# Optimization experiments

Hardware: AMD Instinct MI355X
Metric: run time of the kernel (lower is better)

## Reference

```python
import jax, jax.numpy as jnp
import numpy as np

B, T, C, NH = 4, 2048, 1024, 16
HS = C // NH


def setup_inputs() -> dict:
    key = jax.random.key(0)
    k1, k2, k3, k4, k5 = jax.random.split(key, 5)
    s = 1.0 / np.sqrt(C)
    return {
        "x": jax.random.normal(k1, (B, T, C), dtype=jnp.float32),
        "Wqkv": jax.random.normal(k2, (3 * C, C), dtype=jnp.float32) * s,
        "bqkv": jax.random.normal(k3, (3 * C,), dtype=jnp.float32) * 0.02,
        "Wproj": jax.random.normal(k4, (C, C), dtype=jnp.float32) * s,
        "bproj": jax.random.normal(k5, (C,), dtype=jnp.float32) * 0.02,
    }


def reference(x, Wqkv, bqkv, Wproj, bproj):
    Bsz, Tlen, Cdim = x.shape
    # qkv projection (torch Linear: x @ W.T + b)
    qkv = x @ Wqkv.T + bqkv                      # [B, T, 3C]
    q, k, v = jnp.split(qkv, 3, axis=-1)
    # [B, NH, T, HS]
    q = q.reshape(Bsz, Tlen, NH, HS).transpose(0, 2, 1, 3)
    k = k.reshape(Bsz, Tlen, NH, HS).transpose(0, 2, 1, 3)
    v = v.reshape(Bsz, Tlen, NH, HS).transpose(0, 2, 1, 3)
    scale = 1.0 / np.sqrt(HS)
    att = jnp.einsum('bhqd,bhkd->bhqk', q, k) * scale
    causal = jnp.triu(jnp.ones((Tlen, Tlen), dtype=bool), k=1)
    att = jnp.where(causal[None, None], -jnp.inf, att)
    att = jax.nn.softmax(att, axis=-1)
    y = jnp.einsum('bhqk,bhkd->bhqd', att, v)    # [B, NH, T, HS]
    y = y.transpose(0, 2, 1, 3).reshape(Bsz, Tlen, Cdim)
    return y @ Wproj.T + bproj
```

## Files before the change

kernel.cpp:

```cpp
#include <hip/hip_runtime.h>
#include <hip/hip_bf16.h>

#define B_   4
#define T_   2048
#define C_   1024
#define NH_  16
#define HS_  64
#define M_   8192
#define N1_  3072
#define BH_  64

typedef __attribute__((ext_vector_type(8))) short short8;
typedef __attribute__((ext_vector_type(4))) short short4v;
typedef __attribute__((ext_vector_type(4))) float f32x4;

#define QSCALE 0.18033688011112042f

__device__ __forceinline__ short f2bf(float f) {
  unsigned u = __float_as_uint(f);
  unsigned r = (u + 0x7fffu + ((u >> 16) & 1u)) >> 16;
  return (short)r;
}
__device__ __forceinline__ unsigned pk_bf16(float a, float b) {
  __hip_bfloat162 h = __float22bfloat162_rn(make_float2(a, b));
  union { __hip_bfloat162 h2; unsigned u; } cv; cv.h2 = h; return cv.u;
}

typedef __attribute__((address_space(1))) unsigned int as1_uint;
typedef __attribute__((address_space(3))) unsigned int as3_uint;
__device__ __forceinline__ void g2l16(const void* g, void* l) {
  __builtin_amdgcn_global_load_lds((as1_uint*)g, (as3_uint*)l, 16, 0, 0);
}

__global__ __launch_bounds__(256) void conv_bf16(
    const float* __restrict__ src, short* __restrict__ dst)
{
  const size_t i = ((size_t)blockIdx.x * 256 + threadIdx.x) * 8;
  const f32x4 a = *(const f32x4*)&src[i];
  const f32x4 b = *(const f32x4*)&src[i + 4];
  short8 o;
  o[0] = f2bf(a[0]); o[1] = f2bf(a[1]); o[2] = f2bf(a[2]); o[3] = f2bf(a[3]);
  o[4] = f2bf(b[0]); o[5] = f2bf(b[1]); o[6] = f2bf(b[2]); o[7] = f2bf(b[3]);
  *(short8*)&dst[i] = o;
}

#define NT_ 32

#define GEMM_PRELUDE() \
  const int tid = threadIdx.x; \
  const int lane = tid & 63; \
  const int wid = tid >> 6; \
  const int wy = wid >> 1, wx = wid & 1; \
  const int lq = lane >> 4, lm = lane & 15; \
  const int row0 = blockIdx.x * 128; \
  const int col0 = blockIdx.y * 128; \
  f32x4 acc[4][4] = {}; \
  const int s0 = tid, s1 = tid + 256;             \
  const int r0 = s0 >> 2, r1 = s1 >> 2;           \
  const int c0s = ((s0 & 3) ^ ((r0 >> 1) & 3)) * 8;   \
  const int c1s = ((s1 & 3) ^ ((r1 >> 1) & 3)) * 8; \
  const int rsw = (lq ^ ((lm >> 1) & 3)) * 8;

#define GEMM_STAGE(PA, PB, k0, bi) do { \
    g2l16(&PA[(size_t)(row0 + r0) * C_ + (k0) + c0s], &As[bi][s0 * 8]); \
    g2l16(&PA[(size_t)(row0 + r1) * C_ + (k0) + c1s], &As[bi][s1 * 8]); \
    g2l16(&PB[(size_t)(col0 + r0) * C_ + (k0) + c0s], &Bs[bi][s0 * 8]); \
    g2l16(&PB[(size_t)(col0 + r1) * C_ + (k0) + c1s], &Bs[bi][s1 * 8]); \
  } while (0)

#define GEMM_MAINLOOP(PA, PB) \
  GEMM_STAGE(PA, PB, 0, 0); \
  GEMM_STAGE(PA, PB, 32, 1); \
  int cur = 0; \
  for (int t = 0; t < NT_; ++t) { \
    if (t < NT_ - 1) { asm volatile("s_waitcnt vmcnt(4)" ::: "memory"); } \
    else             { asm volatile("s_waitcnt vmcnt(0)" ::: "memory"); } \
    __builtin_amdgcn_sched_barrier(0); \
    __builtin_amdgcn_s_barrier(); \
    __builtin_amdgcn_sched_barrier(0); \
    { \
      const short* Ab = &As[cur][0]; \
      const short* Bb = &Bs[cur][0]; \
      short8 af[4], bfr[4]; \
      _Pragma("unroll") \
      for (int mi = 0; mi < 4; ++mi) \
        af[mi] = *(const short8*)&Ab[(wy * 64 + mi * 16 + lm) * 32 + rsw]; \
      _Pragma("unroll") \
      for (int ni = 0; ni < 4; ++ni) \
        bfr[ni] = *(const short8*)&Bb[(wx * 64 + ni * 16 + lm) * 32 + rsw]; \
      _Pragma("unroll") \
      for (int mi = 0; mi < 4; ++mi) \
        _Pragma("unroll") \
        for (int ni = 0; ni < 4; ++ni) \
          acc[mi][ni] = __builtin_amdgcn_mfma_f32_16x16x32_bf16(af[mi], bfr[ni], acc[mi][ni], 0, 0, 0); \
    } \
    if (t + 2 < NT_) { \
      const int bi2 = (cur + 2) - ((cur + 2) >= 3 ? 3 : 0); \
      GEMM_STAGE(PA, PB, (t + 2) * 32, bi2); \
    } \
    cur = (cur + 1) - ((cur + 1) >= 3 ? 3 : 0); \
  }

__global__ __launch_bounds__(256) void qkv_gemm(
    const short* __restrict__ X,
    const short* __restrict__ W,
    const float* __restrict__ bias,
    short* __restrict__ Qo, short* __restrict__ Ko, short* __restrict__ Vt)
{
  __shared__ short As[3][128 * 32];
  __shared__ short Bs[3][128 * 32];
  GEMM_PRELUDE();
  GEMM_MAINLOOP(X, W);

#pragma unroll
  for (int ni = 0; ni < 4; ++ni) {
    const int n = col0 + wx * 64 + ni * 16 + lm;
    const float bv = bias[n];
    const int sel = n >> 10;
    const int cc = n & (C_ - 1);
    const int h = cc >> 6, d = cc & 63;
    if (sel == 2) {
#pragma unroll
      for (int mi = 0; mi < 4; ++mi) {
        const int m0 = row0 + wy * 64 + mi * 16 + lq * 4;
        const int b = m0 >> 11, t0 = m0 & (T_ - 1);
        const int bh = b * NH_ + h;
        short4v o;
#pragma unroll
        for (int i = 0; i < 4; ++i) o[i] = f2bf(acc[mi][ni][i] + bv);
        *(short4v*)&Vt[((size_t)bh * HS_ + d) * T_ + t0] = o;
      }
    } else {
      short* dst = (sel == 0) ? Qo : Ko;
      const float qs = (sel == 0) ? QSCALE : 1.0f;
#pragma unroll
      for (int mi = 0; mi < 4; ++mi) {
#pragma unroll
        for (int i = 0; i < 4; ++i) {
          const int m = row0 + wy * 64 + mi * 16 + lq * 4 + i;
          const int b = m >> 11, t = m & (T_ - 1);
          const int bh = b * NH_ + h;
          dst[((size_t)bh * T_ + t) * HS_ + d] = f2bf((acc[mi][ni][i] + bv) * qs);
        }
      }
    }
  }
}

__global__ __launch_bounds__(256) void proj_gemm(
    const short* __restrict__ Y,
    const short* __restrict__ W,
    const float* __restrict__ bias,
    float* __restrict__ Out)
{
  __shared__ short As[3][128 * 32];
  __shared__ short Bs[3][128 * 32];
  GEMM_PRELUDE();
  GEMM_MAINLOOP(Y, W);

#pragma unroll
  for (int ni = 0; ni < 4; ++ni) {
    const int n = col0 + wx * 64 + ni * 16 + lm;
    const float bv = bias[n];
#pragma unroll
    for (int mi = 0; mi < 4; ++mi) {
#pragma unroll
      for (int i = 0; i < 4; ++i) {
        const int m = row0 + wy * 64 + mi * 16 + lq * 4 + i;
        Out[(size_t)m * C_ + n] = acc[mi][ni][i] + bv;
      }
    }
  }
}

#define LDK 72
__global__ __launch_bounds__(512, 4) void attn(
    const short* __restrict__ Qg, const short* __restrict__ Kg,
    const short* __restrict__ Vg, short* __restrict__ Yo)
{
  __shared__ short Ks[64 * LDK];
  __shared__ short Vs[64 * LDK];

  const int tid = threadIdx.x;
  const int lane = tid & 63;
  const int w = tid >> 6;
  const int wq = w & 3;
  const int grp = w >> 2;
  const int lq = lane >> 4, lm = lane & 15;
  const int bh = blockIdx.x;
  const int b = bh >> 4, h = bh & 15;
  const size_t base = (size_t)bh * T_ * HS_;
  const short* __restrict__ Kb = Kg + base;
  const short* __restrict__ Vb = Vg + base;

  const int sr = tid >> 3;
  const int sc = (tid & 7) * 8;

  const int ty = blockIdx.y;
  const int qt = grp ? ty : (15 - ty);
  const int nkt_g = 2 * qt + 2;
  const int nktA = 32 - 2 * ty;

  const int qA = qt * 128 + wq * 16 + lm;
  const int qB = qA + 64;

  const short8 qfA0 = *(const short8*)&Qg[base + (size_t)qA * HS_ + lq * 8];
  const short8 qfA1 = *(const short8*)&Qg[base + (size_t)qA * HS_ + 32 + lq * 8];
  const short8 qfB0 = *(const short8*)&Qg[base + (size_t)qB * HS_ + lq * 8];
  const short8 qfB1 = *(const short8*)&Qg[base + (size_t)qB * HS_ + 32 + lq * 8];

  float lA = 0.0f, lB = 0.0f;
  f32x4 oA[4] = {}, oB[4] = {};

  short8 pk = *(const short8*)&Kb[(size_t)sr * HS_ + sc];
  short8 pv = *(const short8*)&Vb[(size_t)sr * T_ + sc];

#pragma unroll 1
  for (int kt = 0; kt < nktA; ++kt) {
    const int kv0 = kt * 64;

    __syncthreads();
    *(short8*)&Ks[sr * LDK + sc] = pk;
    *(short8*)&Vs[sr * LDK + sc] = pv;
    __syncthreads();

    if (kt + 1 < nktA) {
      pk = *(const short8*)&Kb[(size_t)(kv0 + 64 + sr) * HS_ + sc];
      pv = *(const short8*)&Vb[(size_t)sr * T_ + kv0 + 64 + sc];
    }

    if (kt < nkt_g) {
      const bool doA = (kt <= 2 * qt);

      short8 kf0[4], kf1[4];
#pragma unroll
      for (int ni = 0; ni < 4; ++ni) {
        kf0[ni] = *(const short8*)&Ks[(ni * 16 + lm) * LDK + lq * 8];
        kf1[ni] = *(const short8*)&Ks[(ni * 16 + lm) * LDK + 32 + lq * 8];
      }

      f32x4 svA[4], svB[4];
      if (doA) {
#pragma unroll
        for (int ni = 0; ni < 4; ++ni) {
          f32x4 s = {};
          s = __builtin_amdgcn_mfma_f32_16x16x32_bf16(kf0[ni], qfA0, s, 0, 0, 0);
          svA[ni] = __builtin_amdgcn_mfma_f32_16x16x32_bf16(kf1[ni], qfA1, s, 0, 0, 0);
        }
      }
#pragma unroll
      for (int ni = 0; ni < 4; ++ni) {
        f32x4 s = {};
        s = __builtin_amdgcn_mfma_f32_16x16x32_bf16(kf0[ni], qfB0, s, 0, 0, 0);
        svB[ni] = __builtin_amdgcn_mfma_f32_16x16x32_bf16(kf1[ni], qfB1, s, 0, 0, 0);
      }

      if (kt == 2 * qt) {
#pragma unroll
        for (int ni = 0; ni < 4; ++ni) {
          const int kvb = kv0 + ni * 16 + lq * 4;
#pragma unroll
          for (int i = 0; i < 4; ++i)
            if (kvb + i > qA) svA[ni][i] = -3.0e38f;
        }
      }
      if (kt == 2 * qt + 1) {
#pragma unroll
        for (int ni = 0; ni < 4; ++ni) {
          const int kvb = kv0 + ni * 16 + lq * 4;
#pragma unroll
          for (int i = 0; i < 4; ++i)
            if (kvb + i > qB) svB[ni][i] = -3.0e38f;
        }
      }

      short4v p4A[4], p4B[4];
      if (doA) {
#pragma unroll
        for (int ni = 0; ni < 4; ++ni)
#pragma unroll
          for (int i = 0; i < 4; ++i)
            svA[ni][i] = __builtin_amdgcn_exp2f(svA[ni][i]);
        lA += ((svA[0][0] + svA[0][1]) + (svA[0][2] + svA[0][3]))
            + ((svA[1][0] + svA[1][1]) + (svA[1][2] + svA[1][3]))
            + ((svA[2][0] + svA[2][1]) + (svA[2][2] + svA[2][3]))
            + ((svA[3][0] + svA[3][1]) + (svA[3][2] + svA[3][3]));
#pragma unroll
        for (int ni = 0; ni < 4; ++ni) {
          union { short4v s4; unsigned u[2]; } pk2;
          pk2.u[0] = pk_bf16(svA[ni][0], svA[ni][1]);
          pk2.u[1] = pk_bf16(svA[ni][2], svA[ni][3]);
          p4A[ni] = pk2.s4;
        }
      }
#pragma unroll
      for (int ni = 0; ni < 4; ++ni)
#pragma unroll
        for (int i = 0; i < 4; ++i)
          svB[ni][i] = __builtin_amdgcn_exp2f(svB[ni][i]);
      lB += ((svB[0][0] + svB[0][1]) + (svB[0][2] + svB[0][3]))
          + ((svB[1][0] + svB[1][1]) + (svB[1][2] + svB[1][3]))
          + ((svB[2][0] + svB[2][1]) + (svB[2][2] + svB[2][3]))
          + ((svB[3][0] + svB[3][1]) + (svB[3][2] + svB[3][3]));
#pragma unroll
      for (int ni = 0; ni < 4; ++ni) {
        union { short4v s4; unsigned u[2]; } pk2;
        pk2.u[0] = pk_bf16(svB[ni][0], svB[ni][1]);
        pk2.u[1] = pk_bf16(svB[ni][2], svB[ni][3]);
        p4B[ni] = pk2.s4;
      }

      if (doA) {
#pragma unroll
        for (int di = 0; di < 4; ++di) {
#pragma unroll
          for (int ni = 0; ni < 4; ++ni) {
            const short4v vfr = *(const short4v*)&Vs[(di * 16 + lm) * LDK + ni * 16 + lq * 4];
            oA[di] = __builtin_amdgcn_mfma_f32_16x16x16bf16_1k(vfr, p4A[ni], oA[di], 0, 0, 0);
            oB[di] = __builtin_amdgcn_mfma_f32_16x16x16bf16_1k(vfr, p4B[ni], oB[di], 0, 0, 0);
          }
        }
      } else {
#pragma unroll
        for (int di = 0; di < 4; ++di) {
#pragma unroll
          for (int ni = 0; ni < 4; ++ni) {
            const short4v vfr = *(const short4v*)&Vs[(di * 16 + lm) * LDK + ni * 16 + lq * 4];
            oB[di] = __builtin_amdgcn_mfma_f32_16x16x16bf16_1k(vfr, p4B[ni], oB[di], 0, 0, 0);
          }
        }
      }
    }
  }

  lA += __shfl_xor(lA, 16);
  lA += __shfl_xor(lA, 32);
  lB += __shfl_xor(lB, 16);
  lB += __shfl_xor(lB, 32);
  const float rlA = 1.0f / lA;
  const float rlB = 1.0f / lB;
  const size_t rowA = ((size_t)(b * T_ + qA)) * C_ + h * HS_;
  const size_t rowB = ((size_t)(b * T_ + qB)) * C_ + h * HS_;
#pragma unroll
  for (int di = 0; di < 4; ++di) {
    union { short4v s4; unsigned u[2]; } pk2;
    pk2.u[0] = pk_bf16(oA[di][0] * rlA, oA[di][1] * rlA);
    pk2.u[1] = pk_bf16(oA[di][2] * rlA, oA[di][3] * rlA);
    *(short4v*)&Yo[rowA + di * 16 + lq * 4] = pk2.s4;
    pk2.u[0] = pk_bf16(oB[di][0] * rlB, oB[di][1] * rlB);
    pk2.u[1] = pk_bf16(oB[di][2] * rlB, oB[di][3] * rlB);
    *(short4v*)&Yo[rowB + di * 16 + lq * 4] = pk2.s4;
  }
}

extern "C" void kernel_launch(void* const* d_in, const int* in_sizes, int n_in,
                              void* d_out, int out_size, void* d_ws, size_t ws_size,
                              hipStream_t stream) {
  (void)in_sizes; (void)n_in; (void)out_size;
  const float* x     = (const float*)d_in[0];
  const float* Wqkv  = (const float*)d_in[1];
  const float* bqkv  = (const float*)d_in[2];
  const float* Wproj = (const float*)d_in[3];
  const float* bproj = (const float*)d_in[4];
  float* out = (float*)d_out;

  const size_t nWq = (size_t)N1_ * C_;
  const size_t nWp = (size_t)C_ * C_;
  const size_t nFull = (size_t)M_ * C_;
  const size_t nB = (size_t)T_ * C_;

  dim3 blk(256);
  const size_t need_batched = (nWq + nWp + 4 * nFull) * sizeof(short);

  if (ws_size >= need_batched) {
    short* Wq_bf = (short*)d_ws;
    short* Wp_bf = Wq_bf + nWq;
    short* S0    = Wp_bf + nWp;
    short* Qw    = S0 + nFull;
    short* Kw    = Qw + nFull;
    short* Vw    = Kw + nFull;

    conv_bf16<<<dim3((int)(nWq / 2048)), blk, 0, stream>>>(Wqkv, Wq_bf);
    conv_bf16<<<dim3((int)(nWp / 2048)), blk, 0, stream>>>(Wproj, Wp_bf);
    conv_bf16<<<dim3((int)(nFull / 2048)), blk, 0, stream>>>(x, S0);
    qkv_gemm<<<dim3(M_ / 128, N1_ / 128), blk, 0, stream>>>(S0, Wq_bf, bqkv, Qw, Kw, Vw);
    attn<<<dim3(BH_, 8), dim3(512), 0, stream>>>(Qw, Kw, Vw, S0);
    proj_gemm<<<dim3(M_ / 128, C_ / 128), blk, 0, stream>>>(S0, Wp_bf, bproj, out);
  } else {
    short* Wq_bf = (short*)d_ws;
    short* Wp_bf = Wq_bf + nWq;
    short* S0    = Wp_bf + nWp;
    short* Qw    = S0 + nB;
    short* Kw    = Qw + nB;
    short* Vw    = Kw + nB;

    conv_bf16<<<dim3((int)(nWq / 2048)), blk, 0, stream>>>(Wqkv, Wq_bf);
    conv_bf16<<<dim3((int)(nWp / 2048)), blk, 0, stream>>>(Wproj, Wp_bf);
    for (int b = 0; b < B_; ++b) {
      const float* xb = x   + (size_t)b * nB;
      float*       ob = out + (size_t)b * nB;
      conv_bf16<<<dim3((int)(nB / 2048)), blk, 0, stream>>>(xb, S0);
      qkv_gemm<<<dim3(T_ / 128, N1_ / 128), blk, 0, stream>>>(S0, Wq_bf, bqkv, Qw, Kw, Vw);
      attn<<<dim3(NH_, 8), dim3(512), 0, stream>>>(Qw, Kw, Vw, S0);
      proj_gemm<<<dim3(T_ / 128, C_ / 128), blk, 0, stream>>>(S0, Wp_bf, bproj, ob);
    }
  }
}
```

Before: 248.2 us.

## Widen QKV GEMM tile to 128x256 with 8x4 MFMA per wave

The QKV projection GEMM now uses a 128x256 block tile, with each of four waves covering all 128 rows and a 64-column slice (8x4 MFMA accumulators), instead of 128x128 with a 2x2 wave grid. This raises arithmetic intensity per LDS load and halves the number of blocks that re-read the X tile. In exchange it doubles accumulator registers, raises LDS use, and halves the grid, which may lower occupancy and wave count across the CUs.

```diff
diff --git a/kernel.cpp b/kernel.cpp
--- a/kernel.cpp
+++ b/kernel.cpp
@@ -46,6 +46,111 @@
 
 #define NT_ 32
 
+#define QSTG(bi, k0) do { \
+    _Pragma("unroll") \
+    for (int j = 0; j < 2; ++j) { \
+      const int s = tid + j * 256; \
+      const int r = s >> 2; \
+      const int cc = ((s & 3) ^ ((r >> 1) & 3)) * 8; \
+      g2l16(&X[(size_t)(row0 + r) * C_ + (k0) + cc], &As[bi][s * 8]); \
+    } \
+    _Pragma("unroll") \
+    for (int j = 0; j < 4; ++j) { \
+      const int s = tid + j * 256; \
+      const int r = s >> 2; \
+      const int cc = ((s & 3) ^ ((r >> 1) & 3)) * 8; \
+      g2l16(&W[(size_t)(col0 + r) * C_ + (k0) + cc], &Bs[bi][s * 8]); \
+    } \
+  } while (0)
+
+__global__ __launch_bounds__(256, 2) void qkv_gemm(
+    const short* __restrict__ X,
+    const short* __restrict__ W,
+    const float* __restrict__ bias,
+    short* __restrict__ Qo, short* __restrict__ Ko, short* __restrict__ Vt)
+{
+  __shared__ short As[3][128 * 32];
+  __shared__ short Bs[3][256 * 32];
+  const int tid = threadIdx.x;
+  const int lane = tid & 63;
+  const int wx = tid >> 6;
+  const int lq = lane >> 4, lm = lane & 15;
+  const int row0 = blockIdx.x * 128;
+  const int col0 = blockIdx.y * 256;
+  const int rsw = (lq ^ ((lm >> 1) & 3)) * 8;
+
+  f32x4 acc[8][4] = {};
+
+  QSTG(0, 0);
+  QSTG(1, 32);
+
+  int cur = 0;
+  for (int t = 0; t < NT_; ++t) {
+    if (t < NT_ - 1) { asm volatile("s_waitcnt vmcnt(6)" ::: "memory"); }
+    else             { asm volatile("s_waitcnt vmcnt(0)" ::: "memory"); }
+    __builtin_amdgcn_sched_barrier(0);
+    __builtin_amdgcn_s_barrier();
+    __builtin_amdgcn_sched_barrier(0);
+
+    {
+      const short* Ab = &As[cur][0];
+      const short* Bb = &Bs[cur][0];
+      short8 af[8], bfr[4];
+#pragma unroll
+      for (int mi = 0; mi < 8; ++mi)
+        af[mi] = *(const short8*)&Ab[(mi * 16 + lm) * 32 + rsw];
+#pragma unroll
+      for (int ni = 0; ni < 4; ++ni)
+        bfr[ni] = *(const short8*)&Bb[(wx * 64 + ni * 16 + lm) * 32 + rsw];
+#pragma unroll
+      for (int mi = 0; mi < 8; ++mi)
+#pragma unroll
+        for (int ni = 0; ni < 4; ++ni)
+          acc[mi][ni] = __builtin_amdgcn_mfma_f32_16x16x32_bf16(af[mi], bfr[ni], acc[mi][ni], 0, 0, 0);
+    }
+
+    if (t + 2 < NT_) {
+      const int bi2 = (cur + 2) - ((cur + 2) >= 3 ? 3 : 0);
+      QSTG(bi2, (t + 2) * 32);
+    }
+    cur = (cur + 1) - ((cur + 1) >= 3 ? 3 : 0);
+  }
+
+#pragma unroll
+  for (int ni = 0; ni < 4; ++ni) {
+    const int n = col0 + wx * 64 + ni * 16 + lm;
+    const float bv = bias[n];
+    const int sel = n >> 10;
+    const int cc = n & (C_ - 1);
+    const int h = cc >> 6, d = cc & 63;
+    if (sel == 2) {
+#pragma unroll
+      for (int mi = 0; mi < 8; ++mi) {
+        const int m0 = row0 + mi * 16 + lq * 4;
+        const int b = m0 >> 11, t0 = m0 & (T_ - 1);
+        const int bh = b * NH_ + h;
+        short4v o;
+#pragma unroll
+        for (int i = 0; i < 4; ++i) o[i] = f2bf(acc[mi][ni][i] + bv);
+        *(short4v*)&Vt[((size_t)bh * HS_ + d) * T_ + t0] = o;
+      }
+    } else {
+      short* dst = (sel == 0) ? Qo : Ko;
+      const float qs = (sel == 0) ? QSCALE : 1.0f;
+#pragma unroll
+      for (int mi = 0; mi < 8; ++mi) {
+#pragma unroll
+        for (int i = 0; i < 4; ++i) {
+          const int m = row0 + mi * 16 + lq * 4 + i;
+          const int b = m >> 11, t = m & (T_ - 1);
+          const int bh = b * NH_ + h;
+          dst[((size_t)bh * T_ + t) * HS_ + d] = f2bf((acc[mi][ni][i] + bv) * qs);
+        }
+      }
+    }
+  }
+}
+
 #define GEMM_PRELUDE() \
   const int tid = threadIdx.x; \
   const int lane = tid & 63; \
@@ -55,9 +160,9 @@
   const int row0 = blockIdx.x * 128; \
   const int col0 = blockIdx.y * 128; \
   f32x4 acc[4][4] = {}; \
-  const int s0 = tid, s1 = tid + 256;             \
-  const int r0 = s0 >> 2, r1 = s1 >> 2;           \
-  const int c0s = ((s0 & 3) ^ ((r0 >> 1) & 3)) * 8;   \
+  const int s0 = tid, s1 = tid + 256; \
+  const int r0 = s0 >> 2, r1 = s1 >> 2; \
+  const int c0s = ((s0 & 3) ^ ((r0 >> 1) & 3)) * 8; \
   const int c1s = ((s1 & 3) ^ ((r1 >> 1) & 3)) * 8; \
   const int rsw = (lq ^ ((lm >> 1) & 3)) * 8;
 
@@ -101,52 +206,6 @@
     cur = (cur + 1) - ((cur + 1) >= 3 ? 3 : 0); \
   }
 
-__global__ __launch_bounds__(256) void qkv_gemm(
-    const short* __restrict__ X,
-    const short* __restrict__ W,
-    const float* __restrict__ bias,
-    short* __restrict__ Qo, short* __restrict__ Ko, short* __restrict__ Vt)
-{
-  __shared__ short As[3][128 * 32];
-  __shared__ short Bs[3][128 * 32];
-  GEMM_PRELUDE();
-  GEMM_MAINLOOP(X, W);
-
-#pragma unroll
-  for (int ni = 0; ni < 4; ++ni) {
-    const int n = col0 + wx * 64 + ni * 16 + lm;
-    const float bv = bias[n];
-    const int sel = n >> 10;
-    const int cc = n & (C_ - 1);
-    const int h = cc >> 6, d = cc & 63;
-    if (sel == 2) {
-#pragma unroll
-      for (int mi = 0; mi < 4; ++mi) {
-        const int m0 = row0 + wy * 64 + mi * 16 + lq * 4;
-        const int b = m0 >> 11, t0 = m0 & (T_ - 1);
-        const int bh = b * NH_ + h;
-        short4v o;
-#pragma unroll
-        for (int i = 0; i < 4; ++i) o[i] = f2bf(acc[mi][ni][i] + bv);
-        *(short4v*)&Vt[((size_t)bh * HS_ + d) * T_ + t0] = o;
-      }
-    } else {
-      short* dst = (sel == 0) ? Qo : Ko;
-      const float qs = (sel == 0) ? QSCALE : 1.0f;
-#pragma unroll
-      for (int mi = 0; mi < 4; ++mi) {
-#pragma unroll
-        for (int i = 0; i < 4; ++i) {
-          const int m = row0 + wy * 64 + mi * 16 + lq * 4 + i;
-          const int b = m >> 11, t = m & (T_ - 1);
-          const int bh = b * NH_ + h;
-          dst[((size_t)bh * T_ + t) * HS_ + d] = f2bf((acc[mi][ni][i] + bv) * qs);
-        }
-      }
-    }
-  }
-}
-
 __global__ __launch_bounds__(256) void proj_gemm(
     const short* __restrict__ Y,
     const short* __restrict__ W,
@@ -383,7 +442,7 @@
     conv_bf16<<<dim3((int)(nWq / 2048)), blk, 0, stream>>>(Wqkv, Wq_bf);
     conv_bf16<<<dim3((int)(nWp / 2048)), blk, 0, stream>>>(Wproj, Wp_bf);
     conv_bf16<<<dim3((int)(nFull / 2048)), blk, 0, stream>>>(x, S0);
-    qkv_gemm<<<dim3(M_ / 128, N1_ / 128), blk, 0, stream>>>(S0, Wq_bf, bqkv, Qw, Kw, Vw);
+    qkv_gemm<<<dim3(M_ / 128, N1_ / 256), blk, 0, stream>>>(S0, Wq_bf, bqkv, Qw, Kw, Vw);
     attn<<<dim3(BH_, 8), dim3(512), 0, stream>>>(Qw, Kw, Vw, S0);
     proj_gemm<<<dim3(M_ / 128, C_ / 128), blk, 0, stream>>>(S0, Wp_bf, bproj, out);
   } else {
@@ -400,7 +459,7 @@
       const float* xb = x   + (size_t)b * nB;
       float*       ob = out + (size_t)b * nB;
       conv_bf16<<<dim3((int)(nB / 2048)), blk, 0, stream>>>(xb, S0);
-      qkv_gemm<<<dim3(T_ / 128, N1_ / 128), blk, 0, stream>>>(S0, Wq_bf, bqkv, Qw, Kw, Vw);
+      qkv_gemm<<<dim3(T_ / 128, N1_ / 256), blk, 0, stream>>>(S0, Wq_bf, bqkv, Qw, Kw, Vw);
       attn<<<dim3(NH_, 8), dim3(512), 0, stream>>>(Qw, Kw, Vw, S0);
       proj_gemm<<<dim3(T_ / 128, C_ / 128), blk, 0, stream>>>(S0, Wp_bf, bproj, ob);
     }
```

New measurement: 254.9 us. 1.03x slower.
